# Optimization experiments

Measured on AMD Instinct MI355X. Metric: run time of the kernel, lower is better.

Reference implementation:

```python
import jax, jax.numpy as jnp
import numpy as np

B, L, H, D = 4, 2048, 8, 64


def _combined_mask(Lq):
    # True = masked (disallowed), matching masked_fill_(mask, -inf)
    i = jnp.arange(Lq)[:, None]
    j = jnp.arange(Lq)[None, :]
    diff = i - j
    # log-sparse: query i attends to itself and positions at power-of-2 offsets back
    pow2 = (diff > 0) & ((diff & (diff - 1)) == 0)
    allowed = (diff == 0) | pow2
    log_mask = ~allowed
    causal = j > i  # TriangularCausalMask: strictly-upper triangle masked
    return log_mask | causal  # [Lq, Lq]


def setup_inputs() -> dict:
    key = jax.random.key(0)
    kq, kk, kv = jax.random.split(key, 3)
    return {
        "queries": jax.random.normal(kq, (B, L, H, D), jnp.float32),
        "keys": jax.random.normal(kk, (B, L, H, D), jnp.float32),
        "values": jax.random.normal(kv, (B, L, H, D), jnp.float32),
    }


def reference(queries, keys, values):
    Bq, Lq, Hh, Dd = queries.shape
    scale = 1.0 / jnp.sqrt(jnp.asarray(Dd, queries.dtype))
    # dense scores [B,H,L,L], then structured log-sparse + causal masking
    scores = jnp.einsum('blhd,bshd->bhls', queries, keys)
    mask = _combined_mask(Lq)  # [L,L] True = masked
    scores = jnp.where(mask[None, None, :, :], -jnp.inf, scores)
    A = jax.nn.softmax(scale * scores, axis=-1)  # scale*(-inf) stays -inf
    # dropout is identity in eval mode (reference baseline)
    V = jnp.einsum('bhls,bshd->blhd', A, values)
    return V
```

## Files before the change

kernel.cpp:

```cpp
#include <hip/hip_runtime.h>


typedef float f32x4 __attribute__((ext_vector_type(4)));

constexpr int B = 4, L = 2048, H = 8, D = 64;
constexpr int NPOS = 12;
constexpr int NWG  = (B * L * 2 * 64) / 256;

__global__ __launch_bounds__(256) void logsparse_attn_kernel(
    const float* __restrict__ Q, const float* __restrict__ K,
    const float* __restrict__ V, float* __restrict__ O) {
  const int bid = blockIdx.x;
  const int swz = (bid & 7) * (NWG / 8) + (bid >> 3);
  const int wid = swz * 4 + (int)(threadIdx.x >> 6);
  const int lane = threadIdx.x & 63;
  const int g    = lane >> 4;
  const int dsub = lane & 15;

  const int half = wid >> 13;
  const int bi   = wid & 8191;
  const int i = __builtin_amdgcn_readfirstlane(bi & (L - 1));

  const uint32_t base = ((uint32_t)bi * H + (half * 4 + g)) * D + dsub * 4;

  f32x4 q4 = *reinterpret_cast<const f32x4*>(Q + base);
  const float qs = 0.125f * 1.4426950408889634f;
  q4.x *= qs; q4.y *= qs; q4.z *= qs; q4.w *= qs;

  float sc[NPOS];
  #pragma unroll
  for (int t = 0; t < NPOS; ++t) {
    const int off    = (t == 0) ? 0 : (1 << (t - 1));
    const bool valid = (off <= i);
    const uint32_t kb = base - (uint32_t)(valid ? off * (H * D) : 0);
    const f32x4 k4 = *reinterpret_cast<const f32x4*>(K + kb);
    float p = q4.x * k4.x + q4.y * k4.y + q4.z * k4.z + q4.w * k4.w;
    p += __shfl_xor(p, 1, 64);
    p += __shfl_xor(p, 2, 64);
    p += __shfl_xor(p, 4, 64);
    p += __shfl_xor(p, 8, 64);
    sc[t] = p + (valid ? 0.f : -1e30f);
  }

  const float ma = fmaxf(fmaxf(sc[0], sc[1]), fmaxf(sc[2], sc[3]));
  const float mb = fmaxf(fmaxf(sc[4], sc[5]), fmaxf(sc[6], sc[7]));
  const float mc = fmaxf(fmaxf(sc[8], sc[9]), fmaxf(sc[10], sc[11]));
  const float m  = fmaxf(fmaxf(ma, mb), mc);

  #pragma unroll
  for (int t = 0; t < NPOS; ++t) sc[t] = __builtin_amdgcn_exp2f(sc[t] - m);

  const float sa = (sc[0] + sc[1]) + (sc[2] + sc[3]);
  const float sb = (sc[4] + sc[5]) + (sc[6] + sc[7]);
  const float sd = (sc[8] + sc[9]) + (sc[10] + sc[11]);
  const float inv = __builtin_amdgcn_rcpf(sa + sb + sd);

  f32x4 acc = {0.f, 0.f, 0.f, 0.f};
  #pragma unroll
  for (int t = 0; t < NPOS; ++t) {
    const int off    = (t == 0) ? 0 : (1 << (t - 1));
    const bool valid = (off <= i);
    const uint32_t vb = base - (uint32_t)(valid ? off * (H * D) : 0);
    const f32x4 v4 = *reinterpret_cast<const f32x4*>(V + vb);
    acc.x += sc[t] * v4.x;
    acc.y += sc[t] * v4.y;
    acc.z += sc[t] * v4.z;
    acc.w += sc[t] * v4.w;
  }
  acc.x *= inv; acc.y *= inv; acc.z *= inv; acc.w *= inv;
  __builtin_nontemporal_store(acc, reinterpret_cast<f32x4*>(O + base));
}

extern "C" void kernel_launch(void* const* d_in, const int* in_sizes, int n_in,
                              void* d_out, int out_size, void* d_ws, size_t ws_size,
                              hipStream_t stream) {
  const float* Q = (const float*)d_in[0];
  const float* K = (const float*)d_in[1];
  const float* V = (const float*)d_in[2];
  float* O = (float*)d_out;

  logsparse_attn_kernel<<<NWG, 256, 0, stream>>>(Q, K, V, O);
}
```

Measured before the change: 101.5 us.

## Stage near-window K/V rows in shared memory per strip of queries

Reorganizes work so each workgroup handles a 32-query strip for one (batch, head) and cooperatively loads the preceding 32-row K/V window plus the strip into LDS. The seven near offsets (0..32) read from LDS while the five far offsets (64..1024) are still loaded from global memory, with those far loads issued early. This aims to cut redundant global/L2 traffic for near neighbours shared across queries, at the cost of a barrier, LDS usage and a different workgroup-to-XCD mapping.

Result: faster. 95.05 us (-6.4%).

```diff
diff --git a/kernel.cpp b/kernel.cpp
--- a/kernel.cpp
+++ b/kernel.cpp
@@ -4,71 +4,122 @@
 typedef float f32x4 __attribute__((ext_vector_type(4)));
 
 constexpr int B = 4, L = 2048, H = 8, D = 64;
-constexpr int NPOS = 12;
-constexpr int NWG  = (B * L * 2 * 64) / 256;
+constexpr int STRIP = 32, WIN = 32, LROWS = STRIP + WIN;
+constexpr int NWG = B * H * (L / STRIP);
 
 __global__ __launch_bounds__(256) void logsparse_attn_kernel(
-    const float* __restrict__ Q, const float* __restrict__ K,
-    const float* __restrict__ V, float* __restrict__ O) {
-  const int bid = blockIdx.x;
-  const int swz = (bid & 7) * (NWG / 8) + (bid >> 3);
-  const int wid = swz * 4 + (int)(threadIdx.x >> 6);
-  const int lane = threadIdx.x & 63;
-  const int g    = lane >> 4;
-  const int dsub = lane & 15;
+    const float* __restrict__ Qg, const float* __restrict__ Kg,
+    const float* __restrict__ Vg, float* __restrict__ Og) {
+  __shared__ float Ks[LROWS * D];
+  __shared__ float Vs[LROWS * D];
 
-  const int half = wid >> 13;
-  const int bi   = wid & 8191;
-  const int i = __builtin_amdgcn_readfirstlane(bi & (L - 1));
+  const int bid   = blockIdx.x;
+  const int xcd   = bid & 7;
+  const int kk    = bid >> 3;
+  const int bh    = xcd * 4 + (kk >> 6);
+  const int strip = kk & 63;
+  const int b = bh >> 3, h = bh & 7;
+  const int s = strip * STRIP;
 
-  const uint32_t base = ((uint32_t)bi * H + (half * 4 + g)) * D + dsub * 4;
+  const int tid  = threadIdx.x;
+  const int w    = tid >> 6;
+  const int lane = tid & 63;
+  const int sub  = lane >> 4;
+  const int dl   = lane & 15;
 
-  f32x4 q4 = *reinterpret_cast<const f32x4*>(Q + base);
+  f32x4 kreg[4], vreg[4];
+  int dst[4];
+  #pragma unroll
+  for (int q = 0; q < 4; ++q) {
+    const int r  = w * 16 + q * 4 + sub;
+    const int j  = s - WIN + r;
+    const int jc = j < 0 ? 0 : j;
+    const uint32_t src = (((uint32_t)(b * L + jc)) * H + h) * D + dl * 4;
+    kreg[q] = *(const f32x4*)(Kg + src);
+    vreg[q] = *(const f32x4*)(Vg + src);
+    dst[q]  = r * D + dl * 4;
+  }
+  #pragma unroll
+  for (int q = 0; q < 4; ++q) {
+    *(f32x4*)&Ks[dst[q]] = kreg[q];
+    *(f32x4*)&Vs[dst[q]] = vreg[q];
+  }
+  __syncthreads();
+
   const float qs = 0.125f * 1.4426950408889634f;
-  q4.x *= qs; q4.y *= qs; q4.z *= qs; q4.w *= qs;
-
-  float sc[NPOS];
-  #pragma unroll
-  for (int t = 0; t < NPOS; ++t) {
-    const int off    = (t == 0) ? 0 : (1 << (t - 1));
-    const bool valid = (off <= i);
-    const uint32_t kb = base - (uint32_t)(valid ? off * (H * D) : 0);
-    const f32x4 k4 = *reinterpret_cast<const f32x4*>(K + kb);
-    float p = q4.x * k4.x + q4.y * k4.y + q4.z * k4.z + q4.w * k4.w;
-    p += __shfl_xor(p, 1, 64);
-    p += __shfl_xor(p, 2, 64);
-    p += __shfl_xor(p, 4, 64);
-    p += __shfl_xor(p, 8, 64);
-    sc[t] = p + (valid ? 0.f : -1e30f);
-  }
-
-  const float ma = fmaxf(fmaxf(sc[0], sc[1]), fmaxf(sc[2], sc[3]));
-  const float mb = fmaxf(fmaxf(sc[4], sc[5]), fmaxf(sc[6], sc[7]));
-  const float mc = fmaxf(fmaxf(sc[8], sc[9]), fmaxf(sc[10], sc[11]));
-  const float m  = fmaxf(fmaxf(ma, mb), mc);
 
   #pragma unroll
-  for (int t = 0; t < NPOS; ++t) sc[t] = __builtin_amdgcn_exp2f(sc[t] - m);
+  for (int p = 0; p < 2; ++p) {
+    const int il = w * 8 + p * 4 + sub;
+    const int i  = s + il;
+    const uint32_t qb = (((uint32_t)(b * L + i)) * H + h) * D + dl * 4;
+    f32x4 q4 = *(const f32x4*)(Qg + qb);
 
-  const float sa = (sc[0] + sc[1]) + (sc[2] + sc[3]);
-  const float sb = (sc[4] + sc[5]) + (sc[6] + sc[7]);
-  const float sd = (sc[8] + sc[9]) + (sc[10] + sc[11]);
-  const float inv = __builtin_amdgcn_rcpf(sa + sb + sd);
+    f32x4 kfar[5], vfar[5];
+    #pragma unroll
+    for (int t = 0; t < 5; ++t) {
+      const int off = 64 << t;
+      const int jc  = (off <= i) ? (i - off) : 0;
+      const uint32_t rb = (((uint32_t)(b * L + jc)) * H + h) * D + dl * 4;
+      kfar[t] = *(const f32x4*)(Kg + rb);
+      vfar[t] = *(const f32x4*)(Vg + rb);
+    }
 
-  f32x4 acc = {0.f, 0.f, 0.f, 0.f};
-  #pragma unroll
-  for (int t = 0; t < NPOS; ++t) {
-    const int off    = (t == 0) ? 0 : (1 << (t - 1));
-    const bool valid = (off <= i);
-    const uint32_t vb = base - (uint32_t)(valid ? off * (H * D) : 0);
-    const f32x4 v4 = *reinterpret_cast<const f32x4*>(V + vb);
-    acc.x += sc[t] * v4.x;
-    acc.y += sc[t] * v4.y;
-    acc.z += sc[t] * v4.z;
-    acc.w += sc[t] * v4.w;
+    q4.x *= qs; q4.y *= qs; q4.z *= qs; q4.w *= qs;
+
+    float sc[12];
+    #pragma unroll
+    for (int t = 0; t < 7; ++t) {
+      const int off = (t == 0) ? 0 : (1 << (t - 1));
+      const int r   = il + WIN - off;
+      const f32x4 k4 = *(const f32x4*)&Ks[r * D + dl * 4];
+      float pp = q4.x * k4.x + q4.y * k4.y + q4.z * k4.z + q4.w * k4.w;
+      pp += __shfl_xor(pp, 1, 64);
+      pp += __shfl_xor(pp, 2, 64);
+      pp += __shfl_xor(pp, 4, 64);
+      pp += __shfl_xor(pp, 8, 64);
+      sc[t] = (off <= i) ? pp : -1e30f;
+    }
+    #pragma unroll
+    for (int t = 0; t < 5; ++t) {
+      const int off = 64 << t;
+      float pp = q4.x * kfar[t].x + q4.y * kfar[t].y
+               + q4.z * kfar[t].z + q4.w * kfar[t].w;
+      pp += __shfl_xor(pp, 1, 64);
+      pp += __shfl_xor(pp, 2, 64);
+      pp += __shfl_xor(pp, 4, 64);
+      pp += __shfl_xor(pp, 8, 64);
+      sc[7 + t] = (off <= i) ? pp : -1e30f;
+    }
+
+    const float ma = fmaxf(fmaxf(sc[0], sc[1]), fmaxf(sc[2], sc[3]));
+    const float mb = fmaxf(fmaxf(sc[4], sc[5]), fmaxf(sc[6], sc[7]));
+    const float mc = fmaxf(fmaxf(sc[8], sc[9]), fmaxf(sc[10], sc[11]));
+    const float m  = fmaxf(fmaxf(ma, mb), mc);
+    #pragma unroll
+    for (int t = 0; t < 12; ++t) sc[t] = __builtin_amdgcn_exp2f(sc[t] - m);
+    const float sa = (sc[0] + sc[1]) + (sc[2] + sc[3]);
+    const float sb = (sc[4] + sc[5]) + (sc[6] + sc[7]);
+    const float sd = (sc[8] + sc[9]) + (sc[10] + sc[11]);
+    const float inv = __builtin_amdgcn_rcpf(sa + sb + sd);
+
+    f32x4 acc = {0.f, 0.f, 0.f, 0.f};
+    #pragma unroll
+    for (int t = 0; t < 7; ++t) {
+      const int off = (t == 0) ? 0 : (1 << (t - 1));
+      const int r   = il + WIN - off;
+      const f32x4 v4 = *(const f32x4*)&Vs[r * D + dl * 4];
+      acc.x += sc[t] * v4.x;  acc.y += sc[t] * v4.y;
+      acc.z += sc[t] * v4.z;  acc.w += sc[t] * v4.w;
+    }
+    #pragma unroll
+    for (int t = 0; t < 5; ++t) {
+      acc.x += sc[7 + t] * vfar[t].x;  acc.y += sc[7 + t] * vfar[t].y;
+      acc.z += sc[7 + t] * vfar[t].z;  acc.w += sc[7 + t] * vfar[t].w;
+    }
+    acc.x *= inv; acc.y *= inv; acc.z *= inv; acc.w *= inv;
+    __builtin_nontemporal_store(acc, reinterpret_cast<f32x4*>(Og + qb));
   }
-  acc.x *= inv; acc.y *= inv; acc.z *= inv; acc.w *= inv;
-  __builtin_nontemporal_store(acc, reinterpret_cast<f32x4*>(O + base));
 }
 
 extern "C" void kernel_launch(void* const* d_in, const int* in_sizes, int n_in,
```
